# Optimization experiments

Hardware: AMD Instinct MI355X
Metric: run time of the kernel (lower is better)

Reference implementation:

```python
import jax, jax.numpy as jnp
import numpy as np

IN_CAPS, IN_SIZE = 2401, 8
OUT_CAPS, OUT_SIZE = 8, 16
ROUTING_ITERS = 3


def squash(s, axis):
    mag_sq = jnp.sum(s * s, axis=axis, keepdims=True)
    mag = jnp.sqrt(mag_sq)
    return mag_sq / (1.0 + mag_sq) * (s / mag)


def setup_inputs() -> dict:
    key = jax.random.key(0)
    kx, kw = jax.random.split(key)
    B = 256
    x = jax.random.normal(kx, (B, IN_CAPS, IN_SIZE), dtype=jnp.float32)
    stdv = 1.0 / np.sqrt(IN_CAPS)
    W = jax.random.uniform(kw, (IN_CAPS, OUT_CAPS, OUT_SIZE, IN_SIZE),
                           dtype=jnp.float32, minval=-stdv, maxval=stdv)
    return {"x": x, "W": W}


def reference(x, W):
    # u_hat[b,i,o,c] = W[i,o,c,d] @ x[b,i,d]   -> [B, 2401, 8, 16]
    u_hat = jnp.einsum('iocd,bid->bioc', W, x)
    u_hat_det = jax.lax.stop_gradient(u_hat)

    b_ij = jnp.zeros((IN_CAPS, OUT_CAPS), dtype=x.dtype)
    v_j = None
    for it in range(ROUTING_ITERS):
        c_ij = jax.nn.softmax(b_ij, axis=1)  # softmax over out_capsules
        last = (it == ROUTING_ITERS - 1)
        u = u_hat if last else u_hat_det
        s_j = jnp.einsum('io,bioc->boc', c_ij, u)  # [B, 8, 16]
        v_j = squash(s_j, axis=-1)
        if not last:
            # agreement: mean over batch of <u_hat_i, v_j>
            a = jnp.einsum('bioc,boc->io', u_hat_det, v_j) / x.shape[0]
            b_ij = b_ij + a
    return v_j  # [B, 8, 16]
```

## Files before the change

kernel.cpp:

```cpp
#include <hip/hip_runtime.h>
#include <math.h>

#define IC     2401
#define BSZ    256
#define OC     8
#define CS     16
#define OCC    128
#define XROW   19208
#define KP     19264
#define KTILES 301
#define NI     64

typedef __attribute__((ext_vector_type(8))) short short8;
typedef __attribute__((ext_vector_type(4))) float f32x4;

__device__ __forceinline__ unsigned short f2bf(float f) {
    union { float f; unsigned u; } v; v.f = f;
    const unsigned r = v.u + 0x7FFF + ((v.u >> 16) & 1);
    return (unsigned short)(r >> 16);
}
__device__ __forceinline__ float bf2f(unsigned short h) {
    union { unsigned u; float f; } v; v.u = ((unsigned)h) << 16;
    return v.f;
}

__global__ __launch_bounds__(256)
void prep_kernel(const float* __restrict__ x, const float* __restrict__ W,
                 unsigned short* __restrict__ xT, unsigned short* __restrict__ xB,
                 unsigned short* __restrict__ Wbf, unsigned short* __restrict__ cwt)
{
    const int tid = threadIdx.x;
    if (blockIdx.x < 1204) {
        __shared__ float Ts[64 * 65];
        const int bg = blockIdx.x & 3;
        const int kt = blockIdx.x >> 2;
#pragma unroll
        for (int r = 0; r < 4; ++r) {
            const int flat = r * 256 + tid;
            const int b = flat >> 4, cq = flat & 15;
            const int col = kt * 64 + cq * 4;
            float4 v = make_float4(0.f, 0.f, 0.f, 0.f);
            if (col < XROW) v = *(const float4*)(x + (size_t)(bg * 64 + b) * XROW + col);
            *(float4*)&Ts[b * 65 + cq * 4] = v;
        }
        __syncthreads();
#pragma unroll
        for (int r = 0; r < 2; ++r) {
            const int flat = r * 256 + tid;
            const int rl = flat >> 3, bq = flat & 7;
            union { short8 v; unsigned short h[8]; } o;
#pragma unroll
            for (int j = 0; j < 8; ++j) o.h[j] = f2bf(Ts[(bq * 8 + j) * 65 + rl]);
            *(short8*)(xT + (size_t)(kt * 64 + rl) * 256 + bg * 64 + bq * 8) = o.v;
        }
#pragma unroll
        for (int r = 0; r < 2; ++r) {
            const int flat = r * 256 + tid;
            const int b = flat >> 3, g = flat & 7;
            union { short8 v; unsigned short h[8]; } o;
#pragma unroll
            for (int j = 0; j < 8; ++j) o.h[j] = f2bf(Ts[b * 65 + g * 8 + j]);
            *(short8*)(xB + (size_t)(bg * 64 + b) * KP + (size_t)kt * 64 + g * 8) = o.v;
        }
    } else {
        __shared__ float Ws[8 * 1032];
        const int i0 = (blockIdx.x - 1204) * 8;
#pragma unroll
        for (int r = 0; r < 8; ++r) {
            const int flat = r * 256 + tid;
            const int g = flat >> 8, rem = flat & 255;
            int gi = i0 + g; if (gi > 2400) gi = 2400;
            const float4 v = *(const float4*)(W + (size_t)gi * 1024 + rem * 4);
            *(float4*)&Ws[g * 1032 + rem * 4] = v;
        }
        __syncthreads();
#pragma unroll
        for (int r = 0; r < 4; ++r) {
            const int flat = r * 256 + tid;
            const int oc = flat >> 3, g = flat & 7;
            const int gi = i0 + g;
            union { short8 v; unsigned short h[8]; } w, c;
            if (gi <= 2400) {
                const float* wp = &Ws[g * 1032 + oc * 8];
#pragma unroll
                for (int j = 0; j < 8; ++j) {
                    w.h[j] = f2bf(wp[j]);
                    c.h[j] = f2bf(0.125f * wp[j]);
                }
            } else {
#pragma unroll
                for (int j = 0; j < 8; ++j) { w.h[j] = 0; c.h[j] = 0; }
            }
            *(short8*)(Wbf + (size_t)oc * KP + (size_t)gi * 8) = w.v;
            *(short8*)(cwt + (size_t)oc * KP + (size_t)gi * 8) = c.v;
        }
    }
}

__global__ __launch_bounds__(256, 2)
void s_gemm(const unsigned short* __restrict__ xB, const unsigned short* __restrict__ cwt,
            float* __restrict__ spart)
{
    __shared__ __align__(16) unsigned short Xs[64 * 64];
    __shared__ __align__(16) unsigned short Bs[128 * 64];
    const int tid = threadIdx.x;
    const int bg  = blockIdx.x, iy = blockIdx.y;
    const int b0  = bg * 64;
    const int ln  = tid & 63;
    const int mr  = ln & 15, qd = ln >> 4;
    const int mh  = (tid >> 6) & 1;
    const int nh  = tid >> 7;

    f32x4 acc[2][4];
#pragma unroll
    for (int a = 0; a < 2; ++a)
#pragma unroll
        for (int b = 0; b < 4; ++b) acc[a][b] = (f32x4){0.f, 0.f, 0.f, 0.f};

    for (int kt = iy; kt < KTILES; kt += NI) {
        __syncthreads();
#pragma unroll
        for (int r = 0; r < 2; ++r) {
            const int flat = r * 256 + tid;
            const int b = flat >> 3, col = flat & 7;
            const short8 v = *(const short8*)(xB + (size_t)(b0 + b) * KP + (size_t)(kt * 8 + col) * 8);
            *(short8*)&Xs[b * 64 + ((col ^ (b & 7)) * 8)] = v;
        }
#pragma unroll
        for (int r = 0; r < 4; ++r) {
            const int flat = r * 256 + tid;
            const int oc = flat >> 3, col = flat & 7;
            const short8 w = *(const short8*)(cwt + (size_t)oc * KP + (size_t)(kt * 8 + col) * 8);
            *(short8*)&Bs[oc * 64 + ((col ^ (oc & 7)) * 8)] = w;
        }
        __syncthreads();
#pragma unroll
        for (int kk = 0; kk < 2; ++kk) {
            const int csw = ((kk * 4 + qd) ^ (mr & 7)) * 8;
            const short8 a0 = *(const short8*)&Xs[(mh * 32 + mr) * 64 + csw];
            const short8 a1 = *(const short8*)&Xs[(mh * 32 + 16 + mr) * 64 + csw];
#pragma unroll
            for (int nt = 0; nt < 4; ++nt) {
                const short8 b = *(const short8*)&Bs[(nh * 64 + nt * 16 + mr) * 64 + csw];
                acc[0][nt] = __builtin_amdgcn_mfma_f32_16x16x32_bf16(a0, b, acc[0][nt], 0, 0, 0);
                acc[1][nt] = __builtin_amdgcn_mfma_f32_16x16x32_bf16(a1, b, acc[1][nt], 0, 0, 0);
            }
        }
    }

    float* op = spart + ((size_t)iy * BSZ + b0) * OCC;
#pragma unroll
    for (int mt = 0; mt < 2; ++mt)
#pragma unroll
        for (int nt = 0; nt < 4; ++nt)
#pragma unroll
            for (int r = 0; r < 4; ++r)
                op[(size_t)(mh * 32 + mt * 16 + qd * 4 + r) * OCC + nh * 64 + nt * 16 + mr]
                    = acc[mt][nt][r];
}

__global__ __launch_bounds__(256)
void squash_kernel(const float* __restrict__ spart, float* __restrict__ vout,
                   unsigned short* __restrict__ vT, int writeT)
{
    __shared__ float red[256];
    const int tid = threadIdx.x;
    const int r0  = blockIdx.x * 8;
    const int idx = tid & 127;
    const int k0  = tid >> 7;

    const float* base = spart + (size_t)r0 * 16 + idx;
    float acc = 0.0f;
#pragma unroll 8
    for (int k = k0; k < NI; k += 2) acc += base[(size_t)k * (BSZ * OCC)];
    red[tid] = acc;
    __syncthreads();

    if (tid < 128) {
        const float s = red[tid] + red[tid + 128];
        float ms = s * s;
        ms += __shfl_xor(ms, 1); ms += __shfl_xor(ms, 2);
        ms += __shfl_xor(ms, 4); ms += __shfl_xor(ms, 8);
        const float scale = sqrtf(ms) / (1.0f + ms);
        const float outv = s * scale;
        const int row = r0 + (tid >> 4);
        const int j   = tid & 15;
        if (writeT) {
            vT[(size_t)((row & 7) * 16 + j) * 256 + (row >> 3)] = f2bf(outv);
        } else {
            vout[(size_t)row * 16 + j] = outv;
        }
    }
}

template<bool FIRST>
__global__ __launch_bounds__(256, 2)
void a_gemm(const unsigned short* __restrict__ xT, const unsigned short* __restrict__ vT,
            const unsigned short* __restrict__ Wbf, float* __restrict__ bij,
            unsigned short* __restrict__ cwt)
{
    __shared__ __align__(16) char smraw[128 * 68 * 4];
    unsigned short* As = (unsigned short*)smraw;
    unsigned short* Bx = (unsigned short*)(smraw + 16384);
    float* Hs = (float*)smraw;

    const int tid = threadIdx.x;
    const int i0  = blockIdx.x * 8;
    const int ln  = tid & 63, wv = tid >> 6;
    const int mr  = ln & 15, qd = ln >> 4;

    f32x4 acc[2][4];
#pragma unroll
    for (int a = 0; a < 2; ++a)
#pragma unroll
        for (int b = 0; b < 4; ++b) acc[a][b] = (f32x4){0.f, 0.f, 0.f, 0.f};

    for (int bc = 0; bc < 4; ++bc) {
        __syncthreads();
#pragma unroll
        for (int r = 0; r < 4; ++r) {
            const int flat = r * 256 + tid;
            const int oc = flat >> 3, col = flat & 7;
            const short8 v = *(const short8*)(vT + (size_t)oc * 256 + bc * 64 + col * 8);
            *(short8*)&As[oc * 64 + ((col ^ (oc & 7)) * 8)] = v;
        }
#pragma unroll
        for (int r = 0; r < 2; ++r) {
            const int flat = r * 256 + tid;
            const int rw = flat >> 3, col = flat & 7;
            const short8 v = *(const short8*)(xT + (size_t)(i0 * 8 + rw) * 256 + bc * 64 + col * 8);
            *(short8*)&Bx[rw * 64 + ((col ^ (rw & 7)) * 8)] = v;
        }
        __syncthreads();
#pragma unroll
        for (int kk = 0; kk < 2; ++kk) {
            const int csw = ((kk * 4 + qd) ^ (mr & 7)) * 8;
#pragma unroll
            for (int nt = 0; nt < 4; ++nt) {
                const short8 b = *(const short8*)&Bx[(nt * 16 + mr) * 64 + csw];
#pragma unroll
                for (int mt = 0; mt < 2; ++mt) {
                    const short8 a = *(const short8*)&As[((wv * 2 + mt) * 16 + mr) * 64 + csw];
                    acc[mt][nt] = __builtin_amdgcn_mfma_f32_16x16x32_bf16(a, b, acc[mt][nt], 0, 0, 0);
                }
            }
        }
    }

    __syncthreads();
#pragma unroll
    for (int mt = 0; mt < 2; ++mt)
#pragma unroll
        for (int nt = 0; nt < 4; ++nt)
#pragma unroll
            for (int r = 0; r < 4; ++r)
                Hs[((wv * 2 + mt) * 16 + qd * 4 + r) * 68 + nt * 16 + mr] = acc[mt][nt][r];
    __syncthreads();

    const int ch = tid & 3, oo = (tid >> 2) & 7, il = tid >> 5;
    const int ival = i0 + il;
    const int gi = (ival < IC) ? ival : IC - 1;
    const unsigned short* Wt = Wbf + (size_t)(oo * 16 + ch * 4) * KP + (size_t)gi * 8;

    float wreg[4][8];
#pragma unroll
    for (int c = 0; c < 4; ++c) {
        union { short8 v; unsigned short h[8]; } uw;
        uw.v = *(const short8*)(Wt + (size_t)c * KP);
#pragma unroll
        for (int j = 0; j < 8; ++j) wreg[c][j] = bf2f(uw.h[j]);
    }
    float p = 0.0f;
#pragma unroll
    for (int c = 0; c < 4; ++c) {
        const float* hr = &Hs[(oo * 16 + ch * 4 + c) * 68 + il * 8];
        const float4 h0 = *(const float4*)hr;
        const float4 h1 = *(const float4*)(hr + 4);
        p = fmaf(wreg[c][0], h0.x, p); p = fmaf(wreg[c][1], h0.y, p);
        p = fmaf(wreg[c][2], h0.z, p); p = fmaf(wreg[c][3], h0.w, p);
        p = fmaf(wreg[c][4], h1.x, p); p = fmaf(wreg[c][5], h1.y, p);
        p = fmaf(wreg[c][6], h1.z, p); p = fmaf(wreg[c][7], h1.w, p);
    }
    p += __shfl_xor(p, 1); p += __shfl_xor(p, 2);
    const float anew = p * (1.0f / 256.0f);
    float bv = anew;
    if (!FIRST) bv += bij[gi * 8 + oo];
    float mx = bv;
    mx = fmaxf(mx, __shfl_xor(mx, 4));
    mx = fmaxf(mx, __shfl_xor(mx, 8));
    mx = fmaxf(mx, __shfl_xor(mx, 16));
    const float e = expf(bv - mx);
    float ss = e;
    ss += __shfl_xor(ss, 4); ss += __shfl_xor(ss, 8); ss += __shfl_xor(ss, 16);
    float cv = e / ss;
    if (ival >= IC) cv = 0.0f;
    if (ch == 0 && ival < IC) bij[ival * 8 + oo] = bv;
#pragma unroll
    for (int c = 0; c < 4; ++c) {
        union { short8 v; unsigned short h[8]; } o;
#pragma unroll
        for (int j = 0; j < 8; ++j) o.h[j] = f2bf(cv * wreg[c][j]);
        *(short8*)(cwt + (size_t)(oo * 16 + ch * 4 + c) * KP + (size_t)ival * 8) = o.v;
    }
}

extern "C" void kernel_launch(void* const* d_in, const int* in_sizes, int n_in,
                              void* d_out, int out_size, void* d_ws, size_t ws_size,
                              hipStream_t stream)
{
    const float* x = (const float*)d_in[0];
    const float* W = (const float*)d_in[1];
    float* out = (float*)d_out;

    char* p = (char*)d_ws;
    float*          spart = (float*)p;          p += (size_t)NI * BSZ * OCC * 4;
    unsigned short* xT    = (unsigned short*)p; p += (size_t)KP * 256 * 2;
    unsigned short* xB    = (unsigned short*)p; p += (size_t)256 * KP * 2;
    unsigned short* Wbf   = (unsigned short*)p; p += (size_t)128 * KP * 2;
    unsigned short* cwt   = (unsigned short*)p; p += (size_t)128 * KP * 2;
    unsigned short* vT    = (unsigned short*)p; p += (size_t)128 * 256 * 2;
    float*          bij   = (float*)p;

    const dim3 sgrid(4, NI);

    prep_kernel<<<1505, 256, 0, stream>>>(x, W, xT, xB, Wbf, cwt);

    s_gemm<<<sgrid, 256, 0, stream>>>(xB, cwt, spart);
    squash_kernel<<<256, 256, 0, stream>>>(spart, nullptr, vT, 1);
    a_gemm<true><<<KTILES, 256, 0, stream>>>(xT, vT, Wbf, bij, cwt);
    s_gemm<<<sgrid, 256, 0, stream>>>(xB, cwt, spart);
    squash_kernel<<<256, 256, 0, stream>>>(spart, nullptr, vT, 1);
    a_gemm<false><<<KTILES, 256, 0, stream>>>(xT, vT, Wbf, bij, cwt);
    s_gemm<<<sgrid, 256, 0, stream>>>(xB, cwt, spart);
    squash_kernel<<<256, 256, 0, stream>>>(spart, out, vT, 0);
}
```

Measured before the change: 144.0 us.

## Replace split-K partial buffer with atomics and fuse squash into agreement GEMM

s_gemm now accumulates its split-K partials directly into a zeroed s buffer with float atomics, which removes the separate squash/reduction kernels and the large partial-sum buffer. Each a_gemm block recomputes the squash of the full s (256x128) itself and stages the bf16 v into shared memory. Smaller M tiles (32 rows) double the s_gemm grid. The trade-offs are atomic contention and nondeterministic summation order, plus every a_gemm block redundantly squashing all of s with 64KB of shared memory, which may reduce occupancy.

```diff
diff --git a/kernel.cpp b/kernel.cpp
--- a/kernel.cpp
+++ b/kernel.cpp
@@ -12,6 +12,7 @@
 #define NI     64
 
 typedef __attribute__((ext_vector_type(8))) short short8;
+typedef __attribute__((ext_vector_type(4))) short short4v;
 typedef __attribute__((ext_vector_type(4))) float f32x4;
 
 __device__ __forceinline__ unsigned short f2bf(float f) {
@@ -27,9 +28,13 @@
 __global__ __launch_bounds__(256)
 void prep_kernel(const float* __restrict__ x, const float* __restrict__ W,
                  unsigned short* __restrict__ xT, unsigned short* __restrict__ xB,
-                 unsigned short* __restrict__ Wbf, unsigned short* __restrict__ cwt)
+                 unsigned short* __restrict__ Wbf, unsigned short* __restrict__ cwt,
+                 float* __restrict__ sbuf)
 {
     const int tid = threadIdx.x;
+    if (blockIdx.x < 96)
+        ((float4*)sbuf)[blockIdx.x * 256 + tid] = make_float4(0.f, 0.f, 0.f, 0.f);
+
     if (blockIdx.x < 1204) {
         __shared__ float Ts[64 * 65];
         const int bg = blockIdx.x & 3;
@@ -99,116 +104,107 @@
 
 __global__ __launch_bounds__(256, 2)
 void s_gemm(const unsigned short* __restrict__ xB, const unsigned short* __restrict__ cwt,
-            float* __restrict__ spart)
-{
-    __shared__ __align__(16) unsigned short Xs[64 * 64];
+            float* __restrict__ s)
+{
+    __shared__ __align__(16) unsigned short Xs[32 * 64];
     __shared__ __align__(16) unsigned short Bs[128 * 64];
     const int tid = threadIdx.x;
-    const int bg  = blockIdx.x, iy = blockIdx.y;
-    const int b0  = bg * 64;
+    const int b0  = blockIdx.x * 32;
+    const int iy  = blockIdx.y;
     const int ln  = tid & 63;
     const int mr  = ln & 15, qd = ln >> 4;
-    const int mh  = (tid >> 6) & 1;
-    const int nh  = tid >> 7;
-
-    f32x4 acc[2][4];
-#pragma unroll
-    for (int a = 0; a < 2; ++a)
-#pragma unroll
-        for (int b = 0; b < 4; ++b) acc[a][b] = (f32x4){0.f, 0.f, 0.f, 0.f};
+    const int wv  = tid >> 6;
+    const int mh  = wv & 1;
+    const int nh  = wv >> 1;
+
+    f32x4 acc[4];
+#pragma unroll
+    for (int n = 0; n < 4; ++n) acc[n] = (f32x4){0.f, 0.f, 0.f, 0.f};
 
     for (int kt = iy; kt < KTILES; kt += NI) {
         __syncthreads();
-#pragma unroll
-        for (int r = 0; r < 2; ++r) {
-            const int flat = r * 256 + tid;
-            const int b = flat >> 3, col = flat & 7;
-            const short8 v = *(const short8*)(xB + (size_t)(b0 + b) * KP + (size_t)(kt * 8 + col) * 8);
-            *(short8*)&Xs[b * 64 + ((col ^ (b & 7)) * 8)] = v;
+        {
+            const int b = tid >> 3, g = tid & 7;
+            const short8 v = *(const short8*)(xB + (size_t)(b0 + b) * KP + (size_t)(kt * 8 + g) * 8);
+            *(short8*)&Xs[b * 64 + ((g ^ (b & 7)) * 8)] = v;
         }
 #pragma unroll
         for (int r = 0; r < 4; ++r) {
             const int flat = r * 256 + tid;
-            const int oc = flat >> 3, col = flat & 7;
-            const short8 w = *(const short8*)(cwt + (size_t)oc * KP + (size_t)(kt * 8 + col) * 8);
-            *(short8*)&Bs[oc * 64 + ((col ^ (oc & 7)) * 8)] = w;
+            const int oc = flat >> 3, g = flat & 7;
+            const short8 w = *(const short8*)(cwt + (size_t)oc * KP + (size_t)(kt * 8 + g) * 8);
+            *(short8*)&Bs[oc * 64 + ((g ^ (oc & 7)) * 8)] = w;
         }
         __syncthreads();
 #pragma unroll
         for (int kk = 0; kk < 2; ++kk) {
             const int csw = ((kk * 4 + qd) ^ (mr & 7)) * 8;
-            const short8 a0 = *(const short8*)&Xs[(mh * 32 + mr) * 64 + csw];
-            const short8 a1 = *(const short8*)&Xs[(mh * 32 + 16 + mr) * 64 + csw];
+            const short8 a = *(const short8*)&Xs[(mh * 16 + mr) * 64 + csw];
 #pragma unroll
             for (int nt = 0; nt < 4; ++nt) {
                 const short8 b = *(const short8*)&Bs[(nh * 64 + nt * 16 + mr) * 64 + csw];
-                acc[0][nt] = __builtin_amdgcn_mfma_f32_16x16x32_bf16(a0, b, acc[0][nt], 0, 0, 0);
-                acc[1][nt] = __builtin_amdgcn_mfma_f32_16x16x32_bf16(a1, b, acc[1][nt], 0, 0, 0);
-            }
-        }
-    }
-
-    float* op = spart + ((size_t)iy * BSZ + b0) * OCC;
-#pragma unroll
-    for (int mt = 0; mt < 2; ++mt)
-#pragma unroll
-        for (int nt = 0; nt < 4; ++nt)
-#pragma unroll
-            for (int r = 0; r < 4; ++r)
-                op[(size_t)(mh * 32 + mt * 16 + qd * 4 + r) * OCC + nh * 64 + nt * 16 + mr]
-                    = acc[mt][nt][r];
-}
-
-__global__ __launch_bounds__(256)
-void squash_kernel(const float* __restrict__ spart, float* __restrict__ vout,
-                   unsigned short* __restrict__ vT, int writeT)
-{
-    __shared__ float red[256];
-    const int tid = threadIdx.x;
-    const int r0  = blockIdx.x * 8;
-    const int idx = tid & 127;
-    const int k0  = tid >> 7;
-
-    const float* base = spart + (size_t)r0 * 16 + idx;
-    float acc = 0.0f;
-#pragma unroll 8
-    for (int k = k0; k < NI; k += 2) acc += base[(size_t)k * (BSZ * OCC)];
-    red[tid] = acc;
-    __syncthreads();
-
-    if (tid < 128) {
-        const float s = red[tid] + red[tid + 128];
-        float ms = s * s;
-        ms += __shfl_xor(ms, 1); ms += __shfl_xor(ms, 2);
-        ms += __shfl_xor(ms, 4); ms += __shfl_xor(ms, 8);
-        const float scale = sqrtf(ms) / (1.0f + ms);
-        const float outv = s * scale;
-        const int row = r0 + (tid >> 4);
-        const int j   = tid & 15;
-        if (writeT) {
-            vT[(size_t)((row & 7) * 16 + j) * 256 + (row >> 3)] = f2bf(outv);
-        } else {
-            vout[(size_t)row * 16 + j] = outv;
-        }
-    }
+                acc[nt] = __builtin_amdgcn_mfma_f32_16x16x32_bf16(a, b, acc[nt], 0, 0, 0);
+            }
+        }
+    }
+
+#pragma unroll
+    for (int nt = 0; nt < 4; ++nt)
+#pragma unroll
+        for (int r = 0; r < 4; ++r)
+            unsafeAtomicAdd(&s[(size_t)(b0 + mh * 16 + qd * 4 + r) * OCC + nh * 64 + nt * 16 + mr],
+                            acc[nt][r]);
 }
 
 template<bool FIRST>
 __global__ __launch_bounds__(256, 2)
-void a_gemm(const unsigned short* __restrict__ xT, const unsigned short* __restrict__ vT,
+void a_gemm(const unsigned short* __restrict__ xT, const float* __restrict__ s,
             const unsigned short* __restrict__ Wbf, float* __restrict__ bij,
             unsigned short* __restrict__ cwt)
 {
-    __shared__ __align__(16) char smraw[128 * 68 * 4];
-    unsigned short* As = (unsigned short*)smraw;
-    unsigned short* Bx = (unsigned short*)(smraw + 16384);
-    float* Hs = (float*)smraw;
+    __shared__ __align__(16) unsigned short As[128 * 256];
+    __shared__ __align__(16) unsigned short Bx[64 * 64];
+    float* Hs = (float*)As;
 
     const int tid = threadIdx.x;
     const int i0  = blockIdx.x * 8;
     const int ln  = tid & 63, wv = tid >> 6;
     const int mr  = ln & 15, qd = ln >> 4;
 
+    {
+        const int q = tid & 3, g = tid >> 2;
+        const int gh = g >> 1, gl = g & 1;
+#pragma unroll
+        for (int oh = 0; oh < 2; ++oh) {
+            const int o = q * 2 + oh;
+            float va[4][16];
+            float sc[4];
+#pragma unroll
+            for (int rb = 0; rb < 4; ++rb) {
+                const float4* sr = (const float4*)(s + (size_t)(g * 4 + rb) * OCC + o * 16);
+                const float4 t0 = sr[0], t1 = sr[1], t2 = sr[2], t3 = sr[3];
+                va[rb][0] = t0.x; va[rb][1] = t0.y; va[rb][2]  = t0.z; va[rb][3]  = t0.w;
+                va[rb][4] = t1.x; va[rb][5] = t1.y; va[rb][6]  = t1.z; va[rb][7]  = t1.w;
+                va[rb][8] = t2.x; va[rb][9] = t2.y; va[rb][10] = t2.z; va[rb][11] = t2.w;
+                va[rb][12] = t3.x; va[rb][13] = t3.y; va[rb][14] = t3.z; va[rb][15] = t3.w;
+                float ms = 0.0f;
+#pragma unroll
+                for (int j = 0; j < 16; ++j) ms = fmaf(va[rb][j], va[rb][j], ms);
+                sc[rb] = sqrtf(ms) / (1.0f + ms);
+            }
+#pragma unroll
+            for (int c = 0; c < 16; ++c) {
+                const int oc = o * 16 + c;
+                short4v pk;
+                pk[0] = (short)f2bf(va[0][c] * sc[0]);
+                pk[1] = (short)f2bf(va[1][c] * sc[1]);
+                pk[2] = (short)f2bf(va[2][c] * sc[2]);
+                pk[3] = (short)f2bf(va[3][c] * sc[3]);
+                *(short4v*)&As[oc * 256 + ((gh ^ (oc & 7)) * 8) + gl * 4] = pk;
+            }
+        }
+    }
+
     f32x4 acc[2][4];
 #pragma unroll
     for (int a = 0; a < 2; ++a)
@@ -217,13 +213,6 @@
 
     for (int bc = 0; bc < 4; ++bc) {
         __syncthreads();
-#pragma unroll
-        for (int r = 0; r < 4; ++r) {
-            const int flat = r * 256 + tid;
-            const int oc = flat >> 3, col = flat & 7;
-            const short8 v = *(const short8*)(vT + (size_t)oc * 256 + bc * 64 + col * 8);
-            *(short8*)&As[oc * 64 + ((col ^ (oc & 7)) * 8)] = v;
-        }
 #pragma unroll
         for (int r = 0; r < 2; ++r) {
             const int flat = r * 256 + tid;
@@ -234,15 +223,20 @@
         __syncthreads();
 #pragma unroll
         for (int kk = 0; kk < 2; ++kk) {
+            const int gr  = bc * 8 + kk * 4 + qd;
             const int csw = ((kk * 4 + qd) ^ (mr & 7)) * 8;
+            short8 a[2];
+#pragma unroll
+            for (int mt = 0; mt < 2; ++mt) {
+                const int arow = (wv * 2 + mt) * 16 + mr;
+                a[mt] = *(const short8*)&As[arow * 256 + ((gr ^ (arow & 7)) * 8)];
+            }
 #pragma unroll
             for (int nt = 0; nt < 4; ++nt) {
                 const short8 b = *(const short8*)&Bx[(nt * 16 + mr) * 64 + csw];
 #pragma unroll
-                for (int mt = 0; mt < 2; ++mt) {
-                    const short8 a = *(const short8*)&As[((wv * 2 + mt) * 16 + mr) * 64 + csw];
-                    acc[mt][nt] = __builtin_amdgcn_mfma_f32_16x16x32_bf16(a, b, acc[mt][nt], 0, 0, 0);
-                }
+                for (int mt = 0; mt < 2; ++mt)
+                    acc[mt][nt] = __builtin_amdgcn_mfma_f32_16x16x32_bf16(a[mt], b, acc[mt][nt], 0, 0, 0);
             }
         }
     }
@@ -304,6 +298,29 @@
     }
 }
 
+__global__ __launch_bounds__(256)
+void final_kernel(const float* __restrict__ s, float* __restrict__ out)
+{
+    const int row = blockIdx.x * 256 + threadIdx.x;
+    const float4* p = (const float4*)(s + (size_t)row * CS);
+    const float4 t0 = p[0], t1 = p[1], t2 = p[2], t3 = p[3];
+    float ms = 0.0f;
+    ms = fmaf(t0.x, t0.x, ms); ms = fmaf(t0.y, t0.y, ms);
+    ms = fmaf(t0.z, t0.z, ms); ms = fmaf(t0.w, t0.w, ms);
+    ms = fmaf(t1.x, t1.x, ms); ms = fmaf(t1.y, t1.y, ms);
+    ms = fmaf(t1.z, t1.z, ms); ms = fmaf(t1.w, t1.w, ms);
+    ms = fmaf(t2.x, t2.x, ms); ms = fmaf(t2.y, t2.y, ms);
+    ms = fmaf(t2.z, t2.z, ms); ms = fmaf(t2.w, t2.w, ms);
+    ms = fmaf(t3.x, t3.x, ms); ms = fmaf(t3.y, t3.y, ms);
+    ms = fmaf(t3.z, t3.z, ms); ms = fmaf(t3.w, t3.w, ms);
+    const float sc = sqrtf(ms) / (1.0f + ms);
+    float4* o4 = (float4*)(out + (size_t)row * CS);
+    o4[0] = make_float4(t0.x * sc, t0.y * sc, t0.z * sc, t0.w * sc);
+    o4[1] = make_float4(t1.x * sc, t1.y * sc, t1.z * sc, t1.w * sc);
+    o4[2] = make_float4(t2.x * sc, t2.y * sc, t2.z * sc, t2.w * sc);
+    o4[3] = make_float4(t3.x * sc, t3.y * sc, t3.z * sc, t3.w * sc);
+}
+
 extern "C" void kernel_launch(void* const* d_in, const int* in_sizes, int n_in,
                               void* d_out, int out_size, void* d_ws, size_t ws_size,
                               hipStream_t stream)
@@ -313,24 +330,27 @@
     float* out = (float*)d_out;
 
     char* p = (char*)d_ws;
-    float*          spart = (float*)p;          p += (size_t)NI * BSZ * OCC * 4;
-    unsigned short* xT    = (unsigned short*)p; p += (size_t)KP * 256 * 2;
-    unsigned short* xB    = (unsigned short*)p; p += (size_t)256 * KP * 2;
-    unsigned short* Wbf   = (unsigned short*)p; p += (size_t)128 * KP * 2;
-    unsigned short* cwt   = (unsigned short*)p; p += (size_t)128 * KP * 2;
-    unsigned short* vT    = (unsigned short*)p; p += (size_t)128 * 256 * 2;
-    float*          bij   = (float*)p;
-
-    const dim3 sgrid(4, NI);
-
-    prep_kernel<<<1505, 256, 0, stream>>>(x, W, xT, xB, Wbf, cwt);
-
-    s_gemm<<<sgrid, 256, 0, stream>>>(xB, cwt, spart);
-    squash_kernel<<<256, 256, 0, stream>>>(spart, nullptr, vT, 1);
-    a_gemm<true><<<KTILES, 256, 0, stream>>>(xT, vT, Wbf, bij, cwt);
-    s_gemm<<<sgrid, 256, 0, stream>>>(xB, cwt, spart);
-    squash_kernel<<<256, 256, 0, stream>>>(spart, nullptr, vT, 1);
-    a_gemm<false><<<KTILES, 256, 0, stream>>>(xT, vT, Wbf, bij, cwt);
-    s_gemm<<<sgrid, 256, 0, stream>>>(xB, cwt, spart);
-    squash_kernel<<<256, 256, 0, stream>>>(spart, out, vT, 0);
-}
+    float*          sbuf = (float*)p;           p += 3 * (size_t)BSZ * OCC * 4;
+    unsigned short* xT   = (unsigned short*)p;  p += (size_t)KP * 256 * 2;
+    unsigned short* xB   = (unsigned short*)p;  p += (size_t)256 * KP * 2;
+    unsigned short* Wbf  = (unsigned short*)p;  p += (size_t)128 * KP * 2;
+    unsigned short* cwt  = (unsigned short*)p;  p += (size_t)128 * KP * 2;
+    float*          bij  = (float*)p;
+
+    float* s0 = sbuf;
+    float* s1 = sbuf + (size_t)BSZ * OCC;
+    float* s2 = sbuf + 2 * (size_t)BSZ * OCC;
+
+    const dim3 sgrid(8, NI);
+
+    prep_kernel<<<1505, 256, 0, stream>>>(x, W, xT, xB, Wbf, cwt, sbuf);
+
+    s_gemm<<<sgrid, 256, 0, stream>>>(xB, cwt, s0);
+    a_gemm<true><<<KTILES, 256, 0, stream>>>(xT, s0, Wbf, bij, cwt);
+
+    s_gemm<<<sgrid, 256, 0, stream>>>(xB, cwt, s1);
+    a_gemm<false><<<KTILES, 256, 0, stream>>>(xT, s1, Wbf, bij, cwt);
+
+    s_gemm<<<sgrid, 256, 0, stream>>>(xB, cwt, s2);
+    final_kernel<<<8, 256, 0, stream>>>(s2, out);
+}
```

Result: slower. 157.1 us (+9.1%).

## Fuse squash into split-K GEMM via atomics and last-block reduction

Applied to the files above, without the earlier changes.

The split-K partial buffer and separate squash kernel are replaced. Each GEMM block atomically adds its partials into one small accumulator, and the last block to finish (found through a global counter) performs the squash, writes vT or the output, and re-zeroes the accumulator. This removes three kernel launches and the large partial-sum write/read traffic. The cost is float atomic contention, a serialized tail in which one block squashes all 2048 rows, and a nondeterministic summation order.

```diff
diff --git a/kernel.cpp b/kernel.cpp
--- a/kernel.cpp
+++ b/kernel.cpp
@@ -3,13 +3,12 @@
 
 #define IC     2401
 #define BSZ    256
-#define OC     8
-#define CS     16
 #define OCC    128
 #define XROW   19208
 #define KP     19264
 #define KTILES 301
 #define NI     64
+#define NBLK_S 256
 
 typedef __attribute__((ext_vector_type(8))) short short8;
 typedef __attribute__((ext_vector_type(4))) float f32x4;
@@ -27,9 +26,14 @@
 __global__ __launch_bounds__(256)
 void prep_kernel(const float* __restrict__ x, const float* __restrict__ W,
                  unsigned short* __restrict__ xT, unsigned short* __restrict__ xB,
-                 unsigned short* __restrict__ Wbf, unsigned short* __restrict__ cwt)
+                 unsigned short* __restrict__ Wbf, unsigned short* __restrict__ cwt,
+                 float* __restrict__ sp, unsigned int* __restrict__ counters)
 {
     const int tid = threadIdx.x;
+    if (blockIdx.x < 32)
+        ((float4*)sp)[blockIdx.x * 256 + tid] = make_float4(0.f, 0.f, 0.f, 0.f);
+    if (blockIdx.x == 32 && tid < 3) counters[tid] = 0u;
+
     if (blockIdx.x < 1204) {
         __shared__ float Ts[64 * 65];
         const int bg = blockIdx.x & 3;
@@ -70,8 +74,7 @@
             const int flat = r * 256 + tid;
             const int g = flat >> 8, rem = flat & 255;
             int gi = i0 + g; if (gi > 2400) gi = 2400;
-            const float4 v = *(const float4*)(W + (size_t)gi * 1024 + rem * 4);
-            *(float4*)&Ws[g * 1032 + rem * 4] = v;
+            *(float4*)&Ws[g * 1032 + rem * 4] = *(const float4*)(W + (size_t)gi * 1024 + rem * 4);
         }
         __syncthreads();
 #pragma unroll
@@ -83,10 +86,7 @@
             if (gi <= 2400) {
                 const float* wp = &Ws[g * 1032 + oc * 8];
 #pragma unroll
-                for (int j = 0; j < 8; ++j) {
-                    w.h[j] = f2bf(wp[j]);
-                    c.h[j] = f2bf(0.125f * wp[j]);
-                }
+                for (int j = 0; j < 8; ++j) { w.h[j] = f2bf(wp[j]); c.h[j] = f2bf(0.125f * wp[j]); }
             } else {
 #pragma unroll
                 for (int j = 0; j < 8; ++j) { w.h[j] = 0; c.h[j] = 0; }
@@ -98,11 +98,13 @@
 }
 
 __global__ __launch_bounds__(256, 2)
-void s_gemm(const unsigned short* __restrict__ xB, const unsigned short* __restrict__ cwt,
-            float* __restrict__ spart)
+void sv_kernel(const unsigned short* __restrict__ xB, const unsigned short* __restrict__ cwt,
+               float* __restrict__ sp, unsigned int* __restrict__ counter,
+               unsigned short* __restrict__ vT, float* __restrict__ out, int final_it)
 {
     __shared__ __align__(16) unsigned short Xs[64 * 64];
     __shared__ __align__(16) unsigned short Bs[128 * 64];
+    __shared__ int is_last;
     const int tid = threadIdx.x;
     const int bg  = blockIdx.x, iy = blockIdx.y;
     const int b0  = bg * 64;
@@ -117,6 +119,7 @@
 #pragma unroll
         for (int b = 0; b < 4; ++b) acc[a][b] = (f32x4){0.f, 0.f, 0.f, 0.f};
 
+#pragma unroll 1
     for (int kt = iy; kt < KTILES; kt += NI) {
         __syncthreads();
 #pragma unroll
@@ -148,47 +151,58 @@
         }
     }
 
-    float* op = spart + ((size_t)iy * BSZ + b0) * OCC;
 #pragma unroll
     for (int mt = 0; mt < 2; ++mt)
 #pragma unroll
         for (int nt = 0; nt < 4; ++nt)
 #pragma unroll
             for (int r = 0; r < 4; ++r)
-                op[(size_t)(mh * 32 + mt * 16 + qd * 4 + r) * OCC + nh * 64 + nt * 16 + mr]
-                    = acc[mt][nt][r];
-}
-
-__global__ __launch_bounds__(256)
-void squash_kernel(const float* __restrict__ spart, float* __restrict__ vout,
-                   unsigned short* __restrict__ vT, int writeT)
-{
-    __shared__ float red[256];
-    const int tid = threadIdx.x;
-    const int r0  = blockIdx.x * 8;
-    const int idx = tid & 127;
-    const int k0  = tid >> 7;
-
-    const float* base = spart + (size_t)r0 * 16 + idx;
-    float acc = 0.0f;
-#pragma unroll 8
-    for (int k = k0; k < NI; k += 2) acc += base[(size_t)k * (BSZ * OCC)];
-    red[tid] = acc;
+                unsafeAtomicAdd(&sp[(size_t)(b0 + mh * 32 + mt * 16 + qd * 4 + r) * OCC
+                                    + nh * 64 + nt * 16 + mr], acc[mt][nt][r]);
+
+    __threadfence();
     __syncthreads();
-
-    if (tid < 128) {
-        const float s = red[tid] + red[tid + 128];
-        float ms = s * s;
-        ms += __shfl_xor(ms, 1); ms += __shfl_xor(ms, 2);
-        ms += __shfl_xor(ms, 4); ms += __shfl_xor(ms, 8);
-        const float scale = sqrtf(ms) / (1.0f + ms);
-        const float outv = s * scale;
-        const int row = r0 + (tid >> 4);
-        const int j   = tid & 15;
-        if (writeT) {
-            vT[(size_t)((row & 7) * 16 + j) * 256 + (row >> 3)] = f2bf(outv);
+    if (tid == 0) {
+        const unsigned old = atomicAdd(counter, 1u);
+        is_last = (old == (unsigned)(NBLK_S - 1));
+    }
+    __syncthreads();
+    if (!is_last) return;
+    __threadfence();
+
+#pragma unroll 1
+    for (int rr = 0; rr < 8; ++rr) {
+        const int row = rr * 256 + tid;
+        const float4* pr = (const float4*)(sp + (size_t)row * 16);
+        const float4 t0 = pr[0], t1 = pr[1], t2 = pr[2], t3 = pr[3];
+        float ms = 0.0f;
+        ms = fmaf(t0.x, t0.x, ms); ms = fmaf(t0.y, t0.y, ms);
+        ms = fmaf(t0.z, t0.z, ms); ms = fmaf(t0.w, t0.w, ms);
+        ms = fmaf(t1.x, t1.x, ms); ms = fmaf(t1.y, t1.y, ms);
+        ms = fmaf(t1.z, t1.z, ms); ms = fmaf(t1.w, t1.w, ms);
+        ms = fmaf(t2.x, t2.x, ms); ms = fmaf(t2.y, t2.y, ms);
+        ms = fmaf(t2.z, t2.z, ms); ms = fmaf(t2.w, t2.w, ms);
+        ms = fmaf(t3.x, t3.x, ms); ms = fmaf(t3.y, t3.y, ms);
+        ms = fmaf(t3.z, t3.z, ms); ms = fmaf(t3.w, t3.w, ms);
+        const float sc = sqrtf(ms) / (1.0f + ms);
+        if (final_it) {
+            float4* o4 = (float4*)(out + (size_t)row * 16);
+            o4[0] = make_float4(t0.x * sc, t0.y * sc, t0.z * sc, t0.w * sc);
+            o4[1] = make_float4(t1.x * sc, t1.y * sc, t1.z * sc, t1.w * sc);
+            o4[2] = make_float4(t2.x * sc, t2.y * sc, t2.z * sc, t2.w * sc);
+            o4[3] = make_float4(t3.x * sc, t3.y * sc, t3.z * sc, t3.w * sc);
         } else {
-            vout[(size_t)row * 16 + j] = outv;
+            const int b = row >> 3, o = row & 7;
+            const float vv[16] = { t0.x, t0.y, t0.z, t0.w, t1.x, t1.y, t1.z, t1.w,
+                                   t2.x, t2.y, t2.z, t2.w, t3.x, t3.y, t3.z, t3.w };
+#pragma unroll
+            for (int j = 0; j < 16; ++j)
+                vT[(size_t)(o * 16 + j) * 256 + b] = f2bf(vv[j] * sc);
+            float4* z = (float4*)(sp + (size_t)row * 16);
+            z[0] = make_float4(0.f, 0.f, 0.f, 0.f);
+            z[1] = make_float4(0.f, 0.f, 0.f, 0.f);
+            z[2] = make_float4(0.f, 0.f, 0.f, 0.f);
+            z[3] = make_float4(0.f, 0.f, 0.f, 0.f);
         }
     }
 }
@@ -215,6 +229,7 @@
 #pragma unroll
         for (int b = 0; b < 4; ++b) acc[a][b] = (f32x4){0.f, 0.f, 0.f, 0.f};
 
+#pragma unroll 1
     for (int bc = 0; bc < 4; ++bc) {
         __syncthreads();
 #pragma unroll
@@ -313,24 +328,24 @@
     float* out = (float*)d_out;
 
     char* p = (char*)d_ws;
-    float*          spart = (float*)p;          p += (size_t)NI * BSZ * OCC * 4;
-    unsigned short* xT    = (unsigned short*)p; p += (size_t)KP * 256 * 2;
-    unsigned short* xB    = (unsigned short*)p; p += (size_t)256 * KP * 2;
-    unsigned short* Wbf   = (unsigned short*)p; p += (size_t)128 * KP * 2;
-    unsigned short* cwt   = (unsigned short*)p; p += (size_t)128 * KP * 2;
-    unsigned short* vT    = (unsigned short*)p; p += (size_t)128 * 256 * 2;
-    float*          bij   = (float*)p;
+    float*          sp   = (float*)p;          p += (size_t)BSZ * OCC * 4;
+    unsigned short* xT   = (unsigned short*)p; p += (size_t)KP * 256 * 2;
+    unsigned short* xB   = (unsigned short*)p; p += (size_t)256 * KP * 2;
+    unsigned short* Wbf  = (unsigned short*)p; p += (size_t)128 * KP * 2;
+    unsigned short* cwt  = (unsigned short*)p; p += (size_t)128 * KP * 2;
+    unsigned short* vT   = (unsigned short*)p; p += (size_t)128 * 256 * 2;
+    float*          bij  = (float*)p;          p += (size_t)IC * 8 * 4;
+    unsigned int*   ctr  = (unsigned int*)p;
 
     const dim3 sgrid(4, NI);
 
-    prep_kernel<<<1505, 256, 0, stream>>>(x, W, xT, xB, Wbf, cwt);
-
-    s_gemm<<<sgrid, 256, 0, stream>>>(xB, cwt, spart);
-    squash_kernel<<<256, 256, 0, stream>>>(spart, nullptr, vT, 1);
+    prep_kernel<<<1505, 256, 0, stream>>>(x, W, xT, xB, Wbf, cwt, sp, ctr);
+
+    sv_kernel<<<sgrid, 256, 0, stream>>>(xB, cwt, sp, ctr + 0, vT, out, 0);
     a_gemm<true><<<KTILES, 256, 0, stream>>>(xT, vT, Wbf, bij, cwt);
-    s_gemm<<<sgrid, 256, 0, stream>>>(xB, cwt, spart);
-    squash_kernel<<<256, 256, 0, stream>>>(spart, nullptr, vT, 1);
+
+    sv_kernel<<<sgrid, 256, 0, stream>>>(xB, cwt, sp, ctr + 1, vT, out, 0);
     a_gemm<false><<<KTILES, 256, 0, stream>>>(xT, vT, Wbf, bij, cwt);
-    s_gemm<<<sgrid, 256, 0, stream>>>(xB, cwt, spart);
-    squash_kernel<<<256, 256, 0, stream>>>(spart, out, vT, 0);
-}
+
+    sv_kernel<<<sgrid, 256, 0, stream>>>(xB, cwt, sp, ctr + 2, vT, out, 1);
+}
```

Result: slower. 211.5 us (+46.9%).

## Drop LDS staging in s_gemm; load MFMA fragments directly from global memory

Applied to the files above, without the earlier changes.

The split-K s_gemm kernel no longer stages X and weight tiles through shared memory with barriers. Each wave now owns a 16-row M slice and reads its bf16 A and B fragments straight from global memory into MFMA operands across all 8 N tiles. Dropping the LDS copies and both __syncthreads per K tile removes staging and sync overhead. The cost is redundant global/L2 traffic, since every wave re-reads the same B data with no reuse through LDS. The launch-bounds occupancy hint is relaxed and some loops get unroll 1 pragmas.

```diff
diff --git a/kernel.cpp b/kernel.cpp
--- a/kernel.cpp
+++ b/kernel.cpp
@@ -70,8 +70,7 @@
             const int flat = r * 256 + tid;
             const int g = flat >> 8, rem = flat & 255;
             int gi = i0 + g; if (gi > 2400) gi = 2400;
-            const float4 v = *(const float4*)(W + (size_t)gi * 1024 + rem * 4);
-            *(float4*)&Ws[g * 1032 + rem * 4] = v;
+            *(float4*)&Ws[g * 1032 + rem * 4] = *(const float4*)(W + (size_t)gi * 1024 + rem * 4);
         }
         __syncthreads();
 #pragma unroll
@@ -83,10 +82,7 @@
             if (gi <= 2400) {
                 const float* wp = &Ws[g * 1032 + oc * 8];
 #pragma unroll
-                for (int j = 0; j < 8; ++j) {
-                    w.h[j] = f2bf(wp[j]);
-                    c.h[j] = f2bf(0.125f * wp[j]);
-                }
+                for (int j = 0; j < 8; ++j) { w.h[j] = f2bf(wp[j]); c.h[j] = f2bf(0.125f * wp[j]); }
             } else {
 #pragma unroll
                 for (int j = 0; j < 8; ++j) { w.h[j] = 0; c.h[j] = 0; }
@@ -97,66 +93,45 @@
     }
 }
 
-__global__ __launch_bounds__(256, 2)
+__global__ __launch_bounds__(256)
 void s_gemm(const unsigned short* __restrict__ xB, const unsigned short* __restrict__ cwt,
             float* __restrict__ spart)
 {
-    __shared__ __align__(16) unsigned short Xs[64 * 64];
-    __shared__ __align__(16) unsigned short Bs[128 * 64];
     const int tid = threadIdx.x;
     const int bg  = blockIdx.x, iy = blockIdx.y;
-    const int b0  = bg * 64;
+    const int w   = tid >> 6;
     const int ln  = tid & 63;
     const int mr  = ln & 15, qd = ln >> 4;
-    const int mh  = (tid >> 6) & 1;
-    const int nh  = tid >> 7;
-
-    f32x4 acc[2][4];
-#pragma unroll
-    for (int a = 0; a < 2; ++a)
-#pragma unroll
-        for (int b = 0; b < 4; ++b) acc[a][b] = (f32x4){0.f, 0.f, 0.f, 0.f};
-
+    const int m0  = bg * 64 + w * 16;
+
+    const unsigned short* ap = xB + (size_t)(m0 + mr) * KP + qd * 8;
+    const unsigned short* bp = cwt + (size_t)mr * KP + qd * 8;
+
+    f32x4 acc[8];
+#pragma unroll
+    for (int n = 0; n < 8; ++n) acc[n] = (f32x4){0.f, 0.f, 0.f, 0.f};
+
+#pragma unroll 1
     for (int kt = iy; kt < KTILES; kt += NI) {
-        __syncthreads();
-#pragma unroll
-        for (int r = 0; r < 2; ++r) {
-            const int flat = r * 256 + tid;
-            const int b = flat >> 3, col = flat & 7;
-            const short8 v = *(const short8*)(xB + (size_t)(b0 + b) * KP + (size_t)(kt * 8 + col) * 8);
-            *(short8*)&Xs[b * 64 + ((col ^ (b & 7)) * 8)] = v;
-        }
-#pragma unroll
-        for (int r = 0; r < 4; ++r) {
-            const int flat = r * 256 + tid;
-            const int oc = flat >> 3, col = flat & 7;
-            const short8 w = *(const short8*)(cwt + (size_t)oc * KP + (size_t)(kt * 8 + col) * 8);
-            *(short8*)&Bs[oc * 64 + ((col ^ (oc & 7)) * 8)] = w;
-        }
-        __syncthreads();
+        const int kbase = kt * 64;
 #pragma unroll
         for (int kk = 0; kk < 2; ++kk) {
-            const int csw = ((kk * 4 + qd) ^ (mr & 7)) * 8;
-            const short8 a0 = *(const short8*)&Xs[(mh * 32 + mr) * 64 + csw];
-            const short8 a1 = *(const short8*)&Xs[(mh * 32 + 16 + mr) * 64 + csw];
-#pragma unroll
-            for (int nt = 0; nt < 4; ++nt) {
-                const short8 b = *(const short8*)&Bs[(nh * 64 + nt * 16 + mr) * 64 + csw];
-                acc[0][nt] = __builtin_amdgcn_mfma_f32_16x16x32_bf16(a0, b, acc[0][nt], 0, 0, 0);
-                acc[1][nt] = __builtin_amdgcn_mfma_f32_16x16x32_bf16(a1, b, acc[1][nt], 0, 0, 0);
+            const int k = kbase + kk * 32;
+            const short8 a = *(const short8*)(ap + k);
+#pragma unroll
+            for (int nt = 0; nt < 8; ++nt) {
+                const short8 b = *(const short8*)(bp + (size_t)(nt * 16) * KP + k);
+                acc[nt] = __builtin_amdgcn_mfma_f32_16x16x32_bf16(a, b, acc[nt], 0, 0, 0);
             }
         }
     }
 
-    float* op = spart + ((size_t)iy * BSZ + b0) * OCC;
-#pragma unroll
-    for (int mt = 0; mt < 2; ++mt)
-#pragma unroll
-        for (int nt = 0; nt < 4; ++nt)
-#pragma unroll
-            for (int r = 0; r < 4; ++r)
-                op[(size_t)(mh * 32 + mt * 16 + qd * 4 + r) * OCC + nh * 64 + nt * 16 + mr]
-                    = acc[mt][nt][r];
+    float* op = spart + (size_t)iy * (BSZ * OCC);
+#pragma unroll
+    for (int nt = 0; nt < 8; ++nt)
+#pragma unroll
+        for (int r = 0; r < 4; ++r)
+            op[(size_t)(m0 + qd * 4 + r) * OCC + nt * 16 + mr] = acc[nt][r];
 }
 
 __global__ __launch_bounds__(256)
@@ -215,6 +190,7 @@
 #pragma unroll
         for (int b = 0; b < 4; ++b) acc[a][b] = (f32x4){0.f, 0.f, 0.f, 0.f};
 
+#pragma unroll 1
     for (int bc = 0; bc < 4; ++bc) {
         __syncthreads();
 #pragma unroll
```

Result: slower. 153.3 us (+6.4%).
